# Kernel tuning notes

Hardware: AMD Instinct MI355X
Metric: run time of the kernel (lower is better)

Reference implementation:

```python
import jax, jax.numpy as jnp
import numpy as np

ATTN_BLOCK_SIZE = 4096
NUM_BUCKETS = 64
BUCKET_SIZE = 64
PAST_STEPS = 8
BUCKETS_MINIMUM = 2


def _make_buffers():
    S, B = ATTN_BLOCK_SIZE, NUM_BUCKETS
    idx = np.arange(S)
    arange1 = np.repeat(idx[:, None], S, axis=1)            # [S, S]
    arange2 = ((arange1 - idx[None, :]) % S) // B            # floor-div, nonneg values
    cols = np.arange(B) * B
    arange2 = arange2[:, cols].astype(np.int64)              # [S, B]
    mask = np.tril(np.ones((S, S), dtype=np.float32), k=-BUCKET_SIZE)[:, cols]  # [S, B]
    mask[: BUCKETS_MINIMUM * BUCKET_SIZE] = 0.0
    return arange2, mask


def setup_inputs() -> dict:
    key = jax.random.key(0)
    k1, k2, k3 = jax.random.split(key, 3)
    S, B = ATTN_BLOCK_SIZE, NUM_BUCKETS
    arange2, mask = _make_buffers()
    return {
        "x": jax.random.normal(k1, (16, 16, S, B), dtype=jnp.float32),
        "pb_fwd": jax.random.normal(k2, (1, B), dtype=jnp.float32) * 0.02,
        "pb_bwd": jax.random.normal(k3, (1, B), dtype=jnp.float32) * 0.02,
        "alpha": jnp.ones((1,), dtype=jnp.float32),
        "beta": jnp.full((1,), 0.9, dtype=jnp.float32),
        "arange2": jnp.asarray(arange2),
        "mask": jnp.asarray(mask),
    }


def reference(x, pb_fwd, pb_bwd, alpha, beta, arange2, mask):
    # Training-path forward of Attn_Pred_Model.
    # x: [batch, heads, S, B]; decayed shift-sum over the S (row) axis.
    S = x.shape[-2]
    pad_cfg_tail = [(0, 0)] * (x.ndim - 2)
    result = jnp.zeros_like(x)
    for i in range(PAST_STEPS):  # small fixed unroll, matches torch loop
        shifted = jnp.pad(x[..., : S - (i + 1), :],
                          pad_cfg_tail + [(i + 1, 0), (0, 0)])
        result = result + alpha * (beta ** i) * shifted
    bias_f = pb_fwd[0]                # [B], broadcasts over rows (ones_vec @ param)
    bias_b = pb_bwd[0][arange2]       # gather -> [S, B]
    return (result + bias_f + bias_b) * mask
```

## Files before the change

kernel.cpp:

```cpp
#include <hip/hip_runtime.h>


#define S_DIM 4096
#define PAST 8
#define RROWS 32
#define CHUNK 8
#define STRIPS 16
#define BLOCK_ROWS (RROWS * STRIPS)
#define BLOCKS_PER_PLANE (S_DIM / BLOCK_ROWS)
#define PLANES 256

typedef float v4f __attribute__((ext_vector_type(4)));

#define DO_CHUNK(W, C, rbase)                                               \
    {                                                                       \
        _Pragma("unroll")                                                   \
        for (int d = 0; d < CHUNK; ++d) {                                   \
            v4f acc = c[0] * ((d - 1 >= 0) ? C[d - 1] : W[CHUNK + d - 1]);  \
            _Pragma("unroll")                                               \
            for (int i = 1; i < PAST; ++i) {                                \
                const int idx = d - 1 - i;                                  \
                acc += c[i] * ((idx >= 0) ? C[idx] : W[CHUNK + idx]);       \
            }                                                               \
            op[((rbase) + d) * 16 + j4] = (acc + bias) * mk;                \
        }                                                                   \
    }

__global__ __launch_bounds__(256) void attn_pred_kernel(
    const float* __restrict__ x,
    const float* __restrict__ pb_fwd,
    const float* __restrict__ pb_bwd,
    const float* __restrict__ alpha_p,
    const float* __restrict__ beta_p,
    float* __restrict__ out)
{
    const int j4 = threadIdx.x & 15;
    const int st = threadIdx.x >> 4;
    const int bh = blockIdx.x & (PLANES - 1);
    const int s_slot = blockIdx.x >> 8;
    const int s0 = s_slot * BLOCK_ROWS + st * RROWS;
    const int q  = s0 >> 6;
    const int jb = j4 << 2;

    const size_t plane = (size_t)bh * (S_DIM * 16);
    const v4f* __restrict__ xp = (const v4f*)x + plane;
    v4f* __restrict__       op = (v4f*)out + plane;

    if (s0 < 128 || jb >= q) {
        const v4f z = (v4f){0.f, 0.f, 0.f, 0.f};
        #pragma unroll
        for (int r = 0; r < RROWS; ++r)
            op[(s0 + r) * 16 + j4] = z;
        return;
    }

    const float alpha = alpha_p[0];
    const float beta  = beta_p[0];
    float c[PAST];
    c[0] = alpha;
    #pragma unroll
    for (int i = 1; i < PAST; ++i) c[i] = c[i - 1] * beta;

    const v4f bf = ((const v4f*)pb_fwd)[j4];
    v4f bias;
    bias.x = bf.x + pb_bwd[(q - jb    ) & 63];
    bias.y = bf.y + pb_bwd[(q - jb - 1) & 63];
    bias.z = bf.z + pb_bwd[(q - jb - 2) & 63];
    bias.w = bf.w + pb_bwd[(q - jb - 3) & 63];

    v4f mk;
    mk.x = 1.f;
    mk.y = (jb + 1 < q) ? 1.f : 0.f;
    mk.z = (jb + 2 < q) ? 1.f : 0.f;
    mk.w = (jb + 3 < q) ? 1.f : 0.f;

    v4f A[CHUNK], B[CHUNK];

    #pragma unroll
    for (int k = 0; k < CHUNK; ++k)
        A[k] = xp[(s0 - PAST + k) * 16 + j4];

    #pragma unroll
    for (int k = 0; k < CHUNK; ++k)
        B[k] = xp[(s0 + k) * 16 + j4];
    DO_CHUNK(A, B, s0)

    #pragma unroll
    for (int k = 0; k < CHUNK; ++k)
        A[k] = xp[(s0 + CHUNK + k) * 16 + j4];
    DO_CHUNK(B, A, s0 + CHUNK)

    #pragma unroll
    for (int k = 0; k < CHUNK; ++k)
        B[k] = xp[(s0 + 2 * CHUNK + k) * 16 + j4];
    DO_CHUNK(A, B, s0 + 2 * CHUNK)

    #pragma unroll
    for (int k = 0; k < CHUNK; ++k)
        A[k] = xp[(s0 + 3 * CHUNK + k) * 16 + j4];
    DO_CHUNK(B, A, s0 + 3 * CHUNK)
}

extern "C" void kernel_launch(void* const* d_in, const int* in_sizes, int n_in,
                              void* d_out, int out_size, void* d_ws, size_t ws_size,
                              hipStream_t stream) {
    const float* x       = (const float*)d_in[0];
    const float* pb_fwd  = (const float*)d_in[1];
    const float* pb_bwd  = (const float*)d_in[2];
    const float* alpha_p = (const float*)d_in[3];
    const float* beta_p  = (const float*)d_in[4];
    float* out = (float*)d_out;

    const int grid = PLANES * BLOCKS_PER_PLANE;
    attn_pred_kernel<<<grid, 256, 0, stream>>>(x, pb_fwd, pb_bwd, alpha_p,
                                               beta_p, out);
}
```

Baseline: 498.4 us.

## Remap threads so compute and zero-fill tasks occupy separate wavefronts

Replaces the fixed strip/column thread mapping with a piecewise mapping over (row strip, column chunk) tasks. Tasks that compute the masked decayed sum are packed into the first threads and pure zero-fill tasks into the rest, so wavefronts stay uniform instead of mixing both paths. The aim is to cut branch divergence and idle lanes. In exchange, each group of 4 lanes now covers only 64 contiguous bytes per row, which weakens memory coalescing, and the index arithmetic is hardcoded to these shapes.

```diff
diff --git a/kernel.cpp b/kernel.cpp
--- a/kernel.cpp
+++ b/kernel.cpp
@@ -5,9 +5,6 @@
 #define PAST 8
 #define RROWS 32
 #define CHUNK 8
-#define STRIPS 16
-#define BLOCK_ROWS (RROWS * STRIPS)
-#define BLOCKS_PER_PLANE (S_DIM / BLOCK_ROWS)
 #define PLANES 256
 
 typedef float v4f __attribute__((ext_vector_type(4)));
@@ -15,14 +12,14 @@
 #define DO_CHUNK(W, C, rbase)                                               \
     {                                                                       \
         _Pragma("unroll")                                                   \
-        for (int d = 0; d < CHUNK; ++d) {                                   \
-            v4f acc = c[0] * ((d - 1 >= 0) ? C[d - 1] : W[CHUNK + d - 1]);  \
+        for (int dd = 0; dd < CHUNK; ++dd) {                                \
+            v4f acc = cf[0] * ((dd - 1 >= 0) ? C[dd - 1] : W[CHUNK + dd - 1]); \
             _Pragma("unroll")                                               \
             for (int i = 1; i < PAST; ++i) {                                \
-                const int idx = d - 1 - i;                                  \
-                acc += c[i] * ((idx >= 0) ? C[idx] : W[CHUNK + idx]);       \
+                const int idx = dd - 1 - i;                                 \
+                acc += cf[i] * ((idx >= 0) ? C[idx] : W[CHUNK + idx]);      \
             }                                                               \
-            op[((rbase) + d) * 16 + j4] = (acc + bias) * mk;                \
+            op[((rbase) + dd) * 16 + f4] = (acc + bias) * mk;               \
         }                                                                   \
     }
 
@@ -34,13 +31,37 @@
     const float* __restrict__ beta_p,
     float* __restrict__ out)
 {
-    const int j4 = threadIdx.x & 15;
-    const int st = threadIdx.x >> 4;
     const int bh = blockIdx.x & (PLANES - 1);
-    const int s_slot = blockIdx.x >> 8;
-    const int s0 = s_slot * BLOCK_ROWS + st * RROWS;
+    const int b  = blockIdx.x >> 8;
+    const int T  = (b << 8) | threadIdx.x;
+    const int t  = T >> 2;
+    const int d  = T & 3;
+
+    int s0, c;
+    if (t < 316) {
+        if (t < 28)       { s0 = 128 + (t << 5);                 c = 0; }
+        else if (t < 92)  { const unsigned u = t - 28;
+                            s0 = 128 + ((28 + (u >> 1)) << 5);   c = u & 1; }
+        else if (t < 188) { const unsigned u = t - 92;
+                            const unsigned k3 = u / 3u;
+                            s0 = 128 + ((60 + k3) << 5);         c = u - 3u * k3; }
+        else              { const unsigned u = t - 188;
+                            s0 = 128 + ((92 + (u >> 2)) << 5);   c = u & 3; }
+    } else {
+        const int zt = t - 316;
+        if (zt < 16)       { s0 = (zt >> 2) << 5;                c = zt & 3; }
+        else if (zt < 100) { const unsigned u = zt - 16;
+                             const unsigned k3 = u / 3u;
+                             s0 = 128 + (k3 << 5);               c = 1 + (u - 3u * k3); }
+        else if (zt < 164) { const unsigned u = zt - 100;
+                             s0 = 128 + ((28 + (u >> 1)) << 5);  c = 2 + (u & 1); }
+        else               { const unsigned u = zt - 164;
+                             s0 = 128 + ((60 + u) << 5);         c = 3; }
+    }
+
     const int q  = s0 >> 6;
-    const int jb = j4 << 2;
+    const int f4 = (c << 2) | d;
+    const int jb = f4 << 2;
 
     const size_t plane = (size_t)bh * (S_DIM * 16);
     const v4f* __restrict__ xp = (const v4f*)x + plane;
@@ -50,18 +71,18 @@
         const v4f z = (v4f){0.f, 0.f, 0.f, 0.f};
         #pragma unroll
         for (int r = 0; r < RROWS; ++r)
-            op[(s0 + r) * 16 + j4] = z;
+            op[(s0 + r) * 16 + f4] = z;
         return;
     }
 
     const float alpha = alpha_p[0];
     const float beta  = beta_p[0];
-    float c[PAST];
-    c[0] = alpha;
+    float cf[PAST];
+    cf[0] = alpha;
     #pragma unroll
-    for (int i = 1; i < PAST; ++i) c[i] = c[i - 1] * beta;
+    for (int i = 1; i < PAST; ++i) cf[i] = cf[i - 1] * beta;
 
-    const v4f bf = ((const v4f*)pb_fwd)[j4];
+    const v4f bf = ((const v4f*)pb_fwd)[f4];
     v4f bias;
     bias.x = bf.x + pb_bwd[(q - jb    ) & 63];
     bias.y = bf.y + pb_bwd[(q - jb - 1) & 63];
@@ -78,26 +99,26 @@
 
     #pragma unroll
     for (int k = 0; k < CHUNK; ++k)
-        A[k] = xp[(s0 - PAST + k) * 16 + j4];
+        A[k] = xp[(s0 - PAST + k) * 16 + f4];
 
     #pragma unroll
     for (int k = 0; k < CHUNK; ++k)
-        B[k] = xp[(s0 + k) * 16 + j4];
+        B[k] = xp[(s0 + k) * 16 + f4];
     DO_CHUNK(A, B, s0)
 
     #pragma unroll
     for (int k = 0; k < CHUNK; ++k)
-        A[k] = xp[(s0 + CHUNK + k) * 16 + j4];
+        A[k] = xp[(s0 + CHUNK + k) * 16 + f4];
     DO_CHUNK(B, A, s0 + CHUNK)
 
     #pragma unroll
     for (int k = 0; k < CHUNK; ++k)
-        B[k] = xp[(s0 + 2 * CHUNK + k) * 16 + j4];
+        B[k] = xp[(s0 + 2 * CHUNK + k) * 16 + f4];
     DO_CHUNK(A, B, s0 + 2 * CHUNK)
 
     #pragma unroll
     for (int k = 0; k < CHUNK; ++k)
-        A[k] = xp[(s0 + 3 * CHUNK + k) * 16 + j4];
+        A[k] = xp[(s0 + 3 * CHUNK + k) * 16 + f4];
     DO_CHUNK(B, A, s0 + 3 * CHUNK)
 }
 
@@ -111,7 +132,7 @@
     const float* beta_p  = (const float*)d_in[4];
     float* out = (float*)d_out;
 
-    const int grid = PLANES * BLOCKS_PER_PLANE;
+    const int grid = PLANES * 8;
     attn_pred_kernel<<<grid, 256, 0, stream>>>(x, pb_fwd, pb_bwd, alpha_p,
                                                beta_p, out);
 }
```

Result: slower. 509.2 us (+2.2%).
